# Kernel tuning notes

Hardware: AMD Instinct MI355X
Metric: run time of the kernel (lower is better)

## Reference

```python
import jax, jax.numpy as jnp
import numpy as np

N_SRC = 50000
N_DST = 50000
N_EDGES = 800000
D_IN = 256
NUM_HEADS = 8
OUT_DIM = 16
NEG_SLOPE = 0.2


def setup_inputs() -> dict:
    key = jax.random.key(0)
    ks = jax.random.split(key, 9)
    feat_src = jax.random.normal(ks[0], (N_SRC, D_IN), dtype=jnp.float32)
    feat_dst = jax.random.normal(ks[1], (N_DST, D_IN), dtype=jnp.float32)
    W_src = jax.random.normal(ks[2], (NUM_HEADS * OUT_DIM, D_IN), dtype=jnp.float32) * 0.05
    b_src = jax.random.normal(ks[3], (NUM_HEADS * OUT_DIM,), dtype=jnp.float32) * 0.05
    W_dst = jax.random.normal(ks[4], (NUM_HEADS * OUT_DIM, D_IN), dtype=jnp.float32) * 0.05
    b_dst = jax.random.normal(ks[5], (NUM_HEADS * OUT_DIM,), dtype=jnp.float32) * 0.05
    attn = jax.random.normal(ks[6], (NUM_HEADS, 2 * OUT_DIM), dtype=jnp.float32) * 0.1
    src_idx = jax.random.randint(ks[7], (N_EDGES,), 0, N_SRC, dtype=jnp.int32)
    dst_idx = jax.random.randint(ks[8], (N_EDGES,), 0, N_DST, dtype=jnp.int32)
    return {"feat_src": feat_src, "feat_dst": feat_dst, "W_src": W_src,
            "b_src": b_src, "W_dst": W_dst, "b_dst": b_dst, "attn": attn,
            "src_idx": src_idx, "dst_idx": dst_idx}


def reference(feat_src, feat_dst, W_src, b_src, W_dst, b_dst, attn, src_idx, dst_idx):
    # Node-type-specific linear transforms (feat_drop=0 at inference)
    hs = (feat_src @ W_src.T + b_src).reshape(N_SRC, NUM_HEADS, OUT_DIM)
    hd = (feat_dst @ W_dst.T + b_dst).reshape(N_DST, NUM_HEADS, OUT_DIM)
    # Per-node attention logits: el_i = <hs_i, a_l>, er_j = <hd_j, a_r>
    el = jnp.einsum('nkd,kd->nk', hs, attn[:, :OUT_DIM])  # (N_src, K)
    er = jnp.einsum('nkd,kd->nk', hd, attn[:, OUT_DIM:])  # (N_dst, K)
    # Edge scores: e_uv = LeakyReLU(el_u + er_v)
    e = el[src_idx] + er[dst_idx]                          # (E, K)
    e = jnp.where(e >= 0, e, NEG_SLOPE * e)
    # Edge softmax over incoming edges of each destination node
    m = jax.ops.segment_max(e, dst_idx, num_segments=N_DST)        # (N_dst, K)
    e_exp = jnp.exp(e - m[dst_idx])
    denom = jax.ops.segment_sum(e_exp, dst_idx, num_segments=N_DST)
    a = e_exp / denom[dst_idx]                             # (E, K)
    # Weighted neighbor aggregation: sum_u a_uv * hs_u
    msg = hs[src_idx] * a[:, :, None]                      # (E, K, d_out)
    out = jax.ops.segment_sum(msg, dst_idx, num_segments=N_DST)
    return out.reshape(N_DST, NUM_HEADS * OUT_DIM)
```

## Files before the change

### kernel.cpp

```cpp
#include <hip/hip_runtime.h>
#include <hip/hip_bf16.h>

#define N_SRCC 50000
#define N_DSTC 50000
#define N_EDG 800000
#define NBUK 500
#define DPB 100
#define BCAP 2048
#define EPB 3334
#define NPB 240
#define GEMB 391
#define ERBLK 1024

typedef __attribute__((ext_vector_type(8))) short bf16x8;
typedef __attribute__((ext_vector_type(4))) float f32x4;
typedef __attribute__((ext_vector_type(8))) unsigned short us8;

__device__ inline short f2bf(float x) {
  __hip_bfloat16 b = __float2bfloat16(x);
  return *reinterpret_cast<short*>(&b);
}
__device__ inline float bf2f(unsigned hi16) {
  union { unsigned u; float f; } c; c.u = hi16 << 16; return c.f;
}

__global__ void fold_kernel(const float* __restrict__ Wsrc, const float* __restrict__ bsrc,
                            const float* __restrict__ Wdst, const float* __restrict__ bdst,
                            const float* __restrict__ attn,
                            float* __restrict__ U, float* __restrict__ Cc,
                            short* __restrict__ Wbf, int* __restrict__ bCur) {
  int t = blockIdx.x * blockDim.x + threadIdx.x;
  if (t < 4096) {
    int side = t >> 11;
    int r = (t >> 8) & 7;
    int c = t & 255;
    const float* W = side ? Wdst : Wsrc;
    float s = 0.f;
    #pragma unroll
    for (int d = 0; d < 16; d++)
      s += attn[r*32 + side*16 + d] * W[(r*16 + d)*256 + c];
    U[t] = s;
    const float4* p = (const float4*)&Wsrc[t*8];
    float4 v0 = p[0], v1 = p[1];
    bf16x8 w;
    w[0]=f2bf(v0.x); w[1]=f2bf(v0.y); w[2]=f2bf(v0.z); w[3]=f2bf(v0.w);
    w[4]=f2bf(v1.x); w[5]=f2bf(v1.y); w[6]=f2bf(v1.z); w[7]=f2bf(v1.w);
    *(bf16x8*)&Wbf[t*8] = w;
  }
  if (t < 16) {
    int side = t >> 3, r = t & 7;
    const float* b = side ? bdst : bsrc;
    float s = 0.f;
    #pragma unroll
    for (int d = 0; d < 16; d++) s += attn[r*32 + side*16 + d] * b[r*16 + d];
    Cc[t] = s;
  }
  if (t < NBUK) bCur[t] = 0;
}

__global__ __launch_bounds__(256) void mega(
    const float* __restrict__ feat_src, const float* __restrict__ feat_dst,
    const short* __restrict__ Wbf, const float* __restrict__ bias,
    const float* __restrict__ attn,
    const float* __restrict__ U, const float* __restrict__ Cc,
    const int* __restrict__ src, const int* __restrict__ dst,
    int* __restrict__ bCur, unsigned* __restrict__ bData,
    __hip_bfloat16* __restrict__ hsC, float* __restrict__ el,
    float* __restrict__ er) {
  __shared__ __align__(16) char smem[20480];
  int b = blockIdx.x;
  int t = threadIdx.x;

  if (b < NPB) {
    int* h   = (int*)smem;
    int* cur = (int*)(smem + 2048);
    for (int i = t; i < NBUK; i += 256) h[i] = 0;
    __syncthreads();
    int start = b * EPB;
    int end = min(start + EPB, N_EDG);
    for (int e = start + t; e < end; e += 256)
      atomicAdd(&h[dst[e] / DPB], 1);
    __syncthreads();
    for (int i = t; i < NBUK; i += 256) {
      int c = h[i];
      cur[i] = c ? atomicAdd(&bCur[i], c) : 0;
    }
    __syncthreads();
    for (int e = start + t; e < end; e += 256) {
      int d = dst[e], bk = d / DPB;
      int pos = atomicAdd(&cur[bk], 1);
      if (pos < BCAP)
        bData[(size_t)bk*BCAP + pos] = (unsigned)src[e] | ((unsigned)(d - bk*DPB) << 16);
    }
    return;
  }

  if (b < NPB + GEMB) {
    short (*As)[40] = (short(*)[40])smem;
    short (*Bs)[40] = (short(*)[40])(smem + 10240);
    int lane = t & 63, wid = t >> 6;
    int wr = wid >> 1, wc = wid & 1;
    int row0 = (b - NPB) * 128;
    int lr = lane & 15, lk = lane >> 4;
    int sr = t >> 1, skq = (t & 1) * 16;
    f32x4 acc[4][4] = {};
    for (int k0 = 0; k0 < 256; k0 += 32) {
      {
        int gr = row0 + sr;
        float4 v0 = {}, v1 = {}, v2 = {}, v3 = {};
        if (gr < N_SRCC) {
          const float4* p = (const float4*)&feat_src[(size_t)gr*256 + k0 + skq];
          v0 = p[0]; v1 = p[1]; v2 = p[2]; v3 = p[3];
        }
        bf16x8 t0, t1;
        t0[0]=f2bf(v0.x); t0[1]=f2bf(v0.y); t0[2]=f2bf(v0.z); t0[3]=f2bf(v0.w);
        t0[4]=f2bf(v1.x); t0[5]=f2bf(v1.y); t0[6]=f2bf(v1.z); t0[7]=f2bf(v1.w);
        t1[0]=f2bf(v2.x); t1[1]=f2bf(v2.y); t1[2]=f2bf(v2.z); t1[3]=f2bf(v2.w);
        t1[4]=f2bf(v3.x); t1[5]=f2bf(v3.y); t1[6]=f2bf(v3.z); t1[7]=f2bf(v3.w);
        *(bf16x8*)&As[sr][skq]     = t0;
        *(bf16x8*)&As[sr][skq + 8] = t1;
      }
      *(bf16x8*)&Bs[sr][skq]     = *(const bf16x8*)&Wbf[sr*256 + k0 + skq];
      *(bf16x8*)&Bs[sr][skq + 8] = *(const bf16x8*)&Wbf[sr*256 + k0 + skq + 8];
      __syncthreads();
      bf16x8 af[4], bfr[4];
      #pragma unroll
      for (int m = 0; m < 4; m++)
        af[m] = *(const bf16x8*)&As[wr*64 + m*16 + lr][lk*8];
      #pragma unroll
      for (int n = 0; n < 4; n++)
        bfr[n] = *(const bf16x8*)&Bs[wc*64 + n*16 + lr][lk*8];
      #pragma unroll
      for (int m = 0; m < 4; m++)
        #pragma unroll
        for (int n = 0; n < 4; n++)
          acc[m][n] = __builtin_amdgcn_mfma_f32_16x16x32_bf16(af[m], bfr[n], acc[m][n], 0, 0, 0);
      __syncthreads();
    }
    #pragma unroll
    for (int m = 0; m < 4; m++) {
      int r0 = row0 + wr*64 + m*16 + lk*4;
      #pragma unroll
      for (int n = 0; n < 4; n++) {
        int col = wc*64 + n*16 + lr;
        int h = wc*4 + n;
        float bv = bias[col];
        float al = attn[h*32 + lr];
        #pragma unroll
        for (int j = 0; j < 4; j++) {
          int gr = r0 + j;
          float hv = acc[m][n][j] + bv;
          if (gr < N_SRCC) hsC[(size_t)gr*128 + col] = __float2bfloat16(hv);
          float p = hv * al;
          p += __shfl_xor(p, 1); p += __shfl_xor(p, 2);
          p += __shfl_xor(p, 4); p += __shfl_xor(p, 8);
          if (lr == 0 && gr < N_SRCC) el[gr*8 + h] = p;
        }
      }
    }
    return;
  }

  int w = t >> 6, lane = t & 63;
  int half = lane >> 5, q = lane & 31;
  int wave_id = (b - NPB - GEMB) * 4 + w;
  float4 u0r[8], u1r[8];
  #pragma unroll
  for (int hh = 0; hh < 8; hh++) {
    const float4* up = (const float4*)&U[hh*256 + q*8];
    u0r[hh] = up[0]; u1r[hh] = up[1];
  }
  float cc = (q < 8) ? Cc[q] : 0.f;
  for (int p0 = wave_id; p0 * 2 < N_DSTC; p0 += 4 * ERBLK) {
    int j = p0 * 2 + half;
    const float* fp = &feat_dst[(size_t)j*256 + q*8];
    float4 f0 = *(const float4*)fp;
    float4 f1 = *(const float4*)(fp + 4);
    float p[8];
    #pragma unroll
    for (int hh = 0; hh < 8; hh++) {
      float4 u0 = u0r[hh], u1 = u1r[hh];
      p[hh] = f0.x*u0.x + f0.y*u0.y + f0.z*u0.z + f0.w*u0.w
            + f1.x*u1.x + f1.y*u1.y + f1.z*u1.z + f1.w*u1.w;
    }
    #pragma unroll
    for (int hh = 0; hh < 8; hh++) {
      p[hh] += __shfl_xor(p[hh], 1);  p[hh] += __shfl_xor(p[hh], 2);
      p[hh] += __shfl_xor(p[hh], 4);  p[hh] += __shfl_xor(p[hh], 8);
      p[hh] += __shfl_xor(p[hh], 16);
    }
    if (q < 8) er[j*8 + q] = p[q] + cc;
  }
}

__global__ __launch_bounds__(256) void sort_bucket(const unsigned* __restrict__ bData,
    const int* __restrict__ bCur, int* __restrict__ offS, int* __restrict__ offE,
    unsigned short* __restrict__ srcS) {
  __shared__ int hist[DPB];
  __shared__ int s[128];
  __shared__ int cur[DPB];
  int b = blockIdx.x, t = threadIdx.x;
  int cnt = min(bCur[b], BCAP);
  int base = b * BCAP;
  for (int i = t; i < DPB; i += 256) hist[i] = 0;
  __syncthreads();
  for (int e = t; e < cnt; e += 256) atomicAdd(&hist[bData[base + e] >> 16], 1);
  __syncthreads();
  if (t < 128) s[t] = (t < DPB) ? hist[t] : 0;
  __syncthreads();
  for (int d = 1; d < 128; d <<= 1) {
    int v = (t < 128 && t >= d) ? s[t - d] : 0;
    __syncthreads();
    if (t < 128) s[t] += v;
    __syncthreads();
  }
  if (t < DPB) {
    int excl = s[t] - hist[t];
    cur[t] = excl;
    offS[b * DPB + t] = base + excl;
    offE[b * DPB + t] = base + excl + hist[t];
  }
  __syncthreads();
  for (int e = t; e < cnt; e += 256) {
    unsigned ent = bData[base + e];
    int pos = atomicAdd(&cur[ent >> 16], 1);
    srcS[base + pos] = (unsigned short)(ent & 0xffffu);
  }
}

__global__ __launch_bounds__(256) void aggregate(
    const __hip_bfloat16* __restrict__ hs, const float* __restrict__ el,
    const float* __restrict__ er, const int* __restrict__ offS,
    const int* __restrict__ offE, const unsigned short* __restrict__ srcS,
    float* __restrict__ out) {
  int w = threadIdx.x >> 6;
  int lane = threadIdx.x & 63;
  int jA = blockIdx.x * 8 + w;
  int jB = jA + 4;
  int g = lane >> 4;
  int q = lane & 15;
  int h = q >> 1;
  int e0a = offS[jA], remA = offE[jA] - e0a;
  int e0b = offS[jB], remB = offE[jB] - e0b;
  float erA = er[jA*8 + h];
  float erB = er[jB*8 + h];
  float accA[8] = {}, accB[8] = {};
  float denA = 0.f, denB = 0.f;

  #define AGG_BODY(E, ERH, ACC, DEN) { \
    int s = srcS[E]; \
    float ev = el[s*8 + h] + ERH; \
    ev = ev >= 0.f ? ev : 0.2f * ev; \
    float wg = __expf(ev); \
    DEN += wg; \
    us8 hv = *(const us8*)&hs[(size_t)s*128 + q*8]; \
    _Pragma("unroll") \
    for (int c = 0; c < 8; c++) { \
      ACC[c] = fmaf(wg, bf2f((unsigned)hv[c]), ACC[c]); \
    } \
  }

  int ka = 0, kb = 0;
  while (ka + 8 <= remA && kb + 8 <= remB) {
    AGG_BODY(e0a + ka + g, erA, accA, denA);
    AGG_BODY(e0b + kb + g, erB, accB, denB);
    AGG_BODY(e0a + ka + 4 + g, erA, accA, denA);
    AGG_BODY(e0b + kb + 4 + g, erB, accB, denB);
    ka += 8; kb += 8;
  }
  while (ka + 4 <= remA && kb + 4 <= remB) {
    AGG_BODY(e0a + ka + g, erA, accA, denA);
    AGG_BODY(e0b + kb + g, erB, accB, denB);
    ka += 4; kb += 4;
  }
  while (ka + 4 <= remA) { AGG_BODY(e0a + ka + g, erA, accA, denA); ka += 4; }
  while (kb + 4 <= remB) { AGG_BODY(e0b + kb + g, erB, accB, denB); kb += 4; }
  if (ka + g < remA) AGG_BODY(e0a + ka + g, erA, accA, denA);
  if (kb + g < remB) AGG_BODY(e0b + kb + g, erB, accB, denB);
  #undef AGG_BODY

  #pragma unroll
  for (int c = 0; c < 8; c++) {
    accA[c] += __shfl_xor(accA[c], 16); accA[c] += __shfl_xor(accA[c], 32);
    accB[c] += __shfl_xor(accB[c], 16); accB[c] += __shfl_xor(accB[c], 32);
  }
  denA += __shfl_xor(denA, 16); denA += __shfl_xor(denA, 32);
  denB += __shfl_xor(denB, 16); denB += __shfl_xor(denB, 32);
  if (g == 0) {
    float invA = (remA > 0) ? 1.f / denA : 0.f;
    float invB = (remB > 0) ? 1.f / denB : 0.f;
    float4 r0, r1;
    r0.x = accA[0]*invA; r0.y = accA[1]*invA; r0.z = accA[2]*invA; r0.w = accA[3]*invA;
    r1.x = accA[4]*invA; r1.y = accA[5]*invA; r1.z = accA[6]*invA; r1.w = accA[7]*invA;
    *(float4*)&out[(size_t)jA*128 + q*8]     = r0;
    *(float4*)&out[(size_t)jA*128 + q*8 + 4] = r1;
    r0.x = accB[0]*invB; r0.y = accB[1]*invB; r0.z = accB[2]*invB; r0.w = accB[3]*invB;
    r1.x = accB[4]*invB; r1.y = accB[5]*invB; r1.z = accB[6]*invB; r1.w = accB[7]*invB;
    *(float4*)&out[(size_t)jB*128 + q*8]     = r0;
    *(float4*)&out[(size_t)jB*128 + q*8 + 4] = r1;
  }
}

extern "C" void kernel_launch(void* const* d_in, const int* in_sizes, int n_in,
                              void* d_out, int out_size, void* d_ws, size_t ws_size,
                              hipStream_t stream) {
  const float* feat_src = (const float*)d_in[0];
  const float* feat_dst = (const float*)d_in[1];
  const float* W_src = (const float*)d_in[2];
  const float* b_src = (const float*)d_in[3];
  const float* W_dst = (const float*)d_in[4];
  const float* b_dst = (const float*)d_in[5];
  const float* attn  = (const float*)d_in[6];
  const int* src_idx = (const int*)d_in[7];
  const int* dst_idx = (const int*)d_in[8];
  float* out = (float*)d_out;

  __hip_bfloat16* hs_bf = (__hip_bfloat16*)d_ws;
  float* el = (float*)(hs_bf + (size_t)N_SRCC*128);
  float* er = el + (size_t)N_SRCC*8;
  float* U  = er + (size_t)N_DSTC*8;
  float* Cc = U + 4096;
  short* Wbf = (short*)(Cc + 16);
  int* bCur  = (int*)(Wbf + 32768);
  int* offS  = bCur + NBUK;
  int* offE  = offS + N_DSTC;
  unsigned* bData = (unsigned*)(offE + N_DSTC);
  unsigned short* srcS = (unsigned short*)(bData + (size_t)NBUK*BCAP);

  fold_kernel<<<16, 256, 0, stream>>>(W_src, b_src, W_dst, b_dst, attn, U, Cc, Wbf, bCur);
  mega<<<NPB + GEMB + ERBLK, 256, 0, stream>>>(feat_src, feat_dst, Wbf, b_src, attn,
                                               U + 2048, Cc + 8, src_idx, dst_idx,
                                               bCur, bData, hs_bf, el, er);
  sort_bucket<<<NBUK, 256, 0, stream>>>(bData, bCur, offS, offE, srcS);
  aggregate<<<(N_DSTC + 7)/8, 256, 0, stream>>>(hs_bf, el, er, offS, offE, srcS, out);
}
```

Before: 99.60 us.

## Compute destination attention logits with bf16 MFMA tiles instead of scalar dot products

```diff
diff --git a/kernel.cpp b/kernel.cpp
--- a/kernel.cpp
+++ b/kernel.cpp
@@ -10,7 +10,6 @@
 #define EPB 3334
 #define NPB 240
 #define GEMB 391
-#define ERBLK 1024
 
 typedef __attribute__((ext_vector_type(8))) short bf16x8;
 typedef __attribute__((ext_vector_type(4))) float f32x4;
@@ -28,7 +27,8 @@
                             const float* __restrict__ Wdst, const float* __restrict__ bdst,
                             const float* __restrict__ attn,
                             float* __restrict__ U, float* __restrict__ Cc,
-                            short* __restrict__ Wbf, int* __restrict__ bCur) {
+                            short* __restrict__ Wbf, short* __restrict__ Ubf,
+                            int* __restrict__ bCur) {
   int t = blockIdx.x * blockDim.x + threadIdx.x;
   if (t < 4096) {
     int side = t >> 11;
@@ -40,6 +40,8 @@
     for (int d = 0; d < 16; d++)
       s += attn[r*32 + side*16 + d] * W[(r*16 + d)*256 + c];
     U[t] = s;
+    if (side == 1) Ubf[r*256 + c] = f2bf(s);
+    else           Ubf[2048 + t]  = 0;
     const float4* p = (const float4*)&Wsrc[t*8];
     float4 v0 = p[0], v1 = p[1];
     bf16x8 w;
@@ -60,9 +62,9 @@
 
 __global__ __launch_bounds__(256) void mega(
     const float* __restrict__ feat_src, const float* __restrict__ feat_dst,
-    const short* __restrict__ Wbf, const float* __restrict__ bias,
-    const float* __restrict__ attn,
-    const float* __restrict__ U, const float* __restrict__ Cc,
+    const short* __restrict__ Wbf, const short* __restrict__ Ubf,
+    const float* __restrict__ bias, const float* __restrict__ attn,
+    const float* __restrict__ Cc,
     const int* __restrict__ src, const int* __restrict__ dst,
     int* __restrict__ bCur, unsigned* __restrict__ bData,
     __hip_bfloat16* __restrict__ hsC, float* __restrict__ el,
@@ -161,35 +163,57 @@
     return;
   }
 
-  int w = t >> 6, lane = t & 63;
-  int half = lane >> 5, q = lane & 31;
-  int wave_id = (b - NPB - GEMB) * 4 + w;
-  float4 u0r[8], u1r[8];
-  #pragma unroll
-  for (int hh = 0; hh < 8; hh++) {
-    const float4* up = (const float4*)&U[hh*256 + q*8];
-    u0r[hh] = up[0]; u1r[hh] = up[1];
-  }
-  float cc = (q < 8) ? Cc[q] : 0.f;
-  for (int p0 = wave_id; p0 * 2 < N_DSTC; p0 += 4 * ERBLK) {
-    int j = p0 * 2 + half;
-    const float* fp = &feat_dst[(size_t)j*256 + q*8];
-    float4 f0 = *(const float4*)fp;
-    float4 f1 = *(const float4*)(fp + 4);
-    float p[8];
+  {
+    short (*As)[40]  = (short(*)[40])smem;
+    short (*Bu)[264] = (short(*)[264])(smem + 10240);
+    int lane = t & 63, wid = t >> 6;
+    int row0 = (b - NPB - GEMB) * 128;
+    int lr = lane & 15, lk = lane >> 4;
+    int sr = t >> 1, skq = (t & 1) * 16;
     #pragma unroll
-    for (int hh = 0; hh < 8; hh++) {
-      float4 u0 = u0r[hh], u1 = u1r[hh];
-      p[hh] = f0.x*u0.x + f0.y*u0.y + f0.z*u0.z + f0.w*u0.w
-            + f1.x*u1.x + f1.y*u1.y + f1.z*u1.z + f1.w*u1.w;
-    }
-    #pragma unroll
-    for (int hh = 0; hh < 8; hh++) {
-      p[hh] += __shfl_xor(p[hh], 1);  p[hh] += __shfl_xor(p[hh], 2);
-      p[hh] += __shfl_xor(p[hh], 4);  p[hh] += __shfl_xor(p[hh], 8);
-      p[hh] += __shfl_xor(p[hh], 16);
-    }
-    if (q < 8) er[j*8 + q] = p[q] + cc;
+    for (int i = 0; i < 2; i++) {
+      int c = t + i*256;
+      int r = c >> 5, ck = c & 31;
+      *(bf16x8*)&Bu[r][ck*8] = *(const bf16x8*)&Ubf[r*256 + ck*8];
+    }
+    f32x4 acc[2] = {};
+    for (int k0 = 0; k0 < 256; k0 += 32) {
+      {
+        int gr = row0 + sr;
+        float4 v0 = {}, v1 = {}, v2 = {}, v3 = {};
+        if (gr < N_DSTC) {
+          const float4* p = (const float4*)&feat_dst[(size_t)gr*256 + k0 + skq];
+          v0 = p[0]; v1 = p[1]; v2 = p[2]; v3 = p[3];
+        }
+        bf16x8 t0, t1;
+        t0[0]=f2bf(v0.x); t0[1]=f2bf(v0.y); t0[2]=f2bf(v0.z); t0[3]=f2bf(v0.w);
+        t0[4]=f2bf(v1.x); t0[5]=f2bf(v1.y); t0[6]=f2bf(v1.z); t0[7]=f2bf(v1.w);
+        t1[0]=f2bf(v2.x); t1[1]=f2bf(v2.y); t1[2]=f2bf(v2.z); t1[3]=f2bf(v2.w);
+        t1[4]=f2bf(v3.x); t1[5]=f2bf(v3.y); t1[6]=f2bf(v3.z); t1[7]=f2bf(v3.w);
+        *(bf16x8*)&As[sr][skq]     = t0;
+        *(bf16x8*)&As[sr][skq + 8] = t1;
+      }
+      __syncthreads();
+      bf16x8 bu = *(const bf16x8*)&Bu[lr][k0 + lk*8];
+      #pragma unroll
+      for (int m = 0; m < 2; m++) {
+        bf16x8 af = *(const bf16x8*)&As[wid*32 + m*16 + lr][lk*8];
+        acc[m] = __builtin_amdgcn_mfma_f32_16x16x32_bf16(af, bu, acc[m], 0, 0, 0);
+      }
+      __syncthreads();
+    }
+    if (lr < 8) {
+      float cb = Cc[8 + lr];
+      #pragma unroll
+      for (int m = 0; m < 2; m++) {
+        int r0 = row0 + wid*32 + m*16 + lk*4;
+        #pragma unroll
+        for (int j = 0; j < 4; j++) {
+          int gr = r0 + j;
+          if (gr < N_DSTC) er[gr*8 + lr] = acc[m][j] + cb;
+        }
+      }
+    }
   }
 }
 
@@ -321,16 +345,17 @@
   float* U  = er + (size_t)N_DSTC*8;
   float* Cc = U + 4096;
   short* Wbf = (short*)(Cc + 16);
-  int* bCur  = (int*)(Wbf + 32768);
+  short* Ubf = Wbf + 32768;
+  int* bCur  = (int*)(Ubf + 4096);
   int* offS  = bCur + NBUK;
   int* offE  = offS + N_DSTC;
   unsigned* bData = (unsigned*)(offE + N_DSTC);
   unsigned short* srcS = (unsigned short*)(bData + (size_t)NBUK*BCAP);
 
-  fold_kernel<<<16, 256, 0, stream>>>(W_src, b_src, W_dst, b_dst, attn, U, Cc, Wbf, bCur);
-  mega<<<NPB + GEMB + ERBLK, 256, 0, stream>>>(feat_src, feat_dst, Wbf, b_src, attn,
-                                               U + 2048, Cc + 8, src_idx, dst_idx,
-                                               bCur, bData, hs_bf, el, er);
+  fold_kernel<<<16, 256, 0, stream>>>(W_src, b_src, W_dst, b_dst, attn, U, Cc, Wbf, Ubf, bCur);
+  mega<<<NPB + 2*GEMB, 256, 0, stream>>>(feat_src, feat_dst, Wbf, Ubf, b_src, attn,
+                                         Cc, src_idx, dst_idx, bCur, bData,
+                                         hs_bf, el, er);
   sort_bucket<<<NBUK, 256, 0, stream>>>(bData, bCur, offS, offE, srcS);
   aggregate<<<(N_DSTC + 7)/8, 256, 0, stream>>>(hs_bf, el, er, offS, offE, srcS, out);
 }
```

Measured after the change: 86.60 us. 13.1% less time.
